# Kernel optimization log

Hardware: AMD Instinct MI355X
Metric: run time of the kernel (lower is better)

The kernel has to match this reference:

```python
import jax, jax.numpy as jnp
import numpy as np

ALPHA = 0.2      # LeakyReLU slope
NFEAT = 128
NHID = 8
NHEADS = 8
BN_EPS = 1e-5


def _xavier(k, shape, gain=1.414):
    fan_in, fan_out = shape[-2], shape[-1]
    lim = gain * np.sqrt(6.0 / (fan_in + fan_out))
    return jax.random.uniform(k, shape, jnp.float32, -lim, lim)


def setup_inputs() -> dict:
    key = jax.random.key(0)
    ks = jax.random.split(key, 10)
    B, N = 32, 512
    return {
        "feats": jax.random.normal(ks[0], (B, NFEAT), jnp.float32),
        "neighbor_feats": jax.random.normal(ks[1], (B, N, NFEAT), jnp.float32),
        # per-head GAT params
        "Ws": _xavier(ks[2], (NHEADS, NFEAT, NHID)),
        "As": _xavier(ks[3], (NHEADS, 2 * NHID, 1)),
        # output GAT layer
        "W_out": _xavier(ks[4], (NHID * NHEADS, NHID)),
        "a_out": _xavier(ks[5], (2 * NHID, 1)),
        # classifier: Linear(nfeat+nhid, nhid) -> PReLU -> BN(eval) -> Linear(nhid, 1)
        "lin1_w": _xavier(ks[6], (NHID, NFEAT + NHID), gain=1.0),
        "lin1_b": jnp.zeros((NHID,), jnp.float32),
        "prelu_a": jnp.array(0.25, jnp.float32),
        "bn_gamma": jnp.ones((NHID,), jnp.float32),
        "bn_beta": jnp.zeros((NHID,), jnp.float32),
        "lin2_w": _xavier(ks[7], (1, NHID), gain=1.0),
        "lin2_b": jnp.zeros((1,), jnp.float32),
    }


def _gat_layer(h, W, a, concat):
    # h: (B,N,F), W: (F,D), a: (2D,1)
    Wh = jnp.einsum('bnf,fd->bnd', h, W)            # (B,N,D)
    D = W.shape[1]
    s1 = Wh @ a[:D, 0]                              # (B,N)  a1 . Wh_i
    s2 = Wh @ a[D:, 0]                              # (B,N)  a2 . Wh_j
    # e[b,i,j] = leakyrelu(s1[b,i] + s2[b,j])  == matmul(cat(Wh_i,Wh_j), a)
    e = jax.nn.leaky_relu(s1[:, :, None] + s2[:, None, :], ALPHA)  # (B,N,N)
    att = jax.nn.softmax(e, axis=1)                 # torch F.softmax(e, dim=1)
    h_prime = jnp.einsum('bij,bjd->bid', att, Wh)   # bmm(attention, Wh)
    return jax.nn.elu(h_prime) if concat else h_prime


def reference(feats, neighbor_feats, Ws, As, W_out, a_out,
              lin1_w, lin1_b, prelu_a, bn_gamma, bn_beta, lin2_w, lin2_b):
    # multi-head GAT (dropout is identity in eval mode)
    heads = jax.vmap(lambda W, a: _gat_layer(neighbor_feats, W, a, True))(Ws, As)  # (H,B,N,D)
    H, B, N, D = heads.shape
    x = jnp.moveaxis(heads, 0, 2).reshape(B, N, H * D)  # concat heads along feature dim
    x = jax.nn.elu(_gat_layer(x, W_out, a_out, False))  # (B,N,NHID)
    gat_feats = x[:, 0]                                 # pooling == 'first'
    z = jnp.concatenate([feats, gat_feats], axis=1)     # (B, NFEAT+NHID)
    z = z @ lin1_w.T + lin1_b
    z = jnp.where(z >= 0, z, prelu_a * z)               # PReLU
    # BatchNorm1d in eval mode with running mean=0, var=1
    z = z / jnp.sqrt(1.0 + BN_EPS) * bn_gamma + bn_beta
    out = z @ lin2_w.T + lin2_b                         # (B,1)
    return out.squeeze(1)
```

## Files before the change

kernel.cpp:

```cpp
#include <hip/hip_runtime.h>
#include <math.h>

#define BB 32
#define NN 512
#define NFEAT 128
#define NHID 8
#define NHEADS 8
#define LALPHA 0.2f

__device__ __forceinline__ float elu1(float x)  { return x > 0.f ? x : __expf(x) - 1.f; }

__device__ __forceinline__ unsigned ordkey(float v) {
    unsigned u = __float_as_uint(v);
    return u ^ (((unsigned)((int)u >> 31)) | 0x80000000u);
}
__device__ __forceinline__ float unord(unsigned k) {
    unsigned u = (k & 0x80000000u) ? (k ^ 0x80000000u) : ~k;
    return __uint_as_float(u);
}

#if __has_builtin(__builtin_amdgcn_update_dpp)
__device__ __forceinline__ float wscan(float x, int lane) {
    int y;
    y = __builtin_amdgcn_update_dpp(0, __float_as_int(x), 0x111, 0xF, 0xF, true); x += __int_as_float(y);
    y = __builtin_amdgcn_update_dpp(0, __float_as_int(x), 0x112, 0xF, 0xF, true); x += __int_as_float(y);
    y = __builtin_amdgcn_update_dpp(0, __float_as_int(x), 0x114, 0xF, 0xF, true); x += __int_as_float(y);
    y = __builtin_amdgcn_update_dpp(0, __float_as_int(x), 0x118, 0xF, 0xF, true); x += __int_as_float(y);
    y = __builtin_amdgcn_update_dpp(0, __float_as_int(x), 0x142, 0xA, 0xF, true); x += __int_as_float(y);
    y = __builtin_amdgcn_update_dpp(0, __float_as_int(x), 0x143, 0xC, 0xF, true); x += __int_as_float(y);
    return x;
}
#else
__device__ __forceinline__ float wscan(float x, int lane) {
    #pragma unroll
    for (int s = 1; s < 64; s <<= 1) {
        float y = __shfl_up(x, (unsigned)s, 64);
        x += (lane >= s) ? y : 0.f;
    }
    return x;
}
#endif

__device__ __forceinline__ unsigned long long shflxor64(unsigned long long x, int j) {
    unsigned lo = (unsigned)__shfl_xor((int)(unsigned)x, j, 64);
    unsigned hw = (unsigned)__shfl_xor((int)(unsigned)(x >> 32), j, 64);
    return (((unsigned long long)hw) << 32) | lo;
}

__device__ __forceinline__ int lb512u64(const unsigned long long* a, unsigned long long v) {
    int lo = 0;
    #pragma unroll
    for (int s = NN / 2; s >= 1; s >>= 1)
        if (a[lo + s - 1] < v) lo += s;
    return lo;
}

__device__ __forceinline__ unsigned long long sortnet512(
        unsigned long long x, unsigned long long* lds, int r, bool active) {
    #pragma unroll
    for (int k = 2; k <= NN; k <<= 1) {
        #pragma unroll
        for (int j = k >> 1; j >= 1; j >>= 1) {
            unsigned long long y;
            if (j >= 64) {
                if (active) lds[r] = x;
                __syncthreads();
                y = active ? lds[r ^ j] : 0ull;
                __syncthreads();
            } else {
                y = shflxor64(x, j);
            }
            if (active) {
                const bool takeMin = ((r & j) == 0) == ((r & k) == 0);
                const bool sw = takeMin ? (y < x) : (x < y);
                x = sw ? y : x;
            }
        }
    }
    if (active) lds[r] = x;
    __syncthreads();
    return x;
}

__global__ __launch_bounds__(1024) void k12_gat1(
        const float* __restrict__ nf, const float* __restrict__ Ws,
        const float* __restrict__ As, float* __restrict__ x)
{
    __shared__ __align__(16) float WT[NHID * NFEAT];
    __shared__ float aL[16];
    __shared__ __align__(16) float whL[NN][NHID];
    __shared__ __align__(16) float part[NN][NHID];
    __shared__ __align__(16) unsigned long long key1L[NN];
    __shared__ __align__(16) unsigned long long key2L[NN];
    __shared__ float prefP[NN], prefQ[NN], denS[NN];
    __shared__ __align__(16) float PP[NN][NHID];
    __shared__ __align__(16) float QQ[NN][NHID];
    __shared__ __align__(16) float wvT[16][NHID];

    const int blk = blockIdx.x;
    const int b = blk & 31, h = blk >> 5;
    const int t = threadIdx.x;
    const int r = t & (NN - 1);
    const bool hi = t >= NN;
    const int lane = t & 63, w = t >> 6;

    {
        const int f = t >> 3, d = t & 7;
        WT[d * NFEAT + f] = Ws[(size_t)h * NFEAT * NHID + t];
    }
    if (t < 16) aL[t] = As[h * 16 + t];
    __syncthreads();

    float acc[NHID];
    {
        #pragma unroll
        for (int d = 0; d < NHID; ++d) acc[d] = 0.f;
        const float4* row = (const float4*)(nf + ((size_t)b * NN + r) * NFEAT + (hi ? 64 : 0));
        const int fb = hi ? 16 : 0;
        const float4* WT4 = (const float4*)WT;
        #pragma unroll 4
        for (int f4 = 0; f4 < 16; ++f4) {
            float4 v = row[f4];
            #pragma unroll
            for (int d = 0; d < NHID; ++d) {
                float4 wv = WT4[d * 32 + fb + f4];
                acc[d] += v.x * wv.x + v.y * wv.y + v.z * wv.z + v.w * wv.w;
            }
        }
        if (hi) {
            float4* pp = (float4*)&part[r][0];
            pp[0] = make_float4(acc[0], acc[1], acc[2], acc[3]);
            pp[1] = make_float4(acc[4], acc[5], acc[6], acc[7]);
        }
    }
    __syncthreads();

    float v1 = 0.f;
    unsigned long long sk = 0ull;
    if (!hi) {
        #pragma unroll
        for (int d = 0; d < NHID; ++d) acc[d] += part[t][d];
        float a1 = 0.f, a2 = 0.f;
        #pragma unroll
        for (int d = 0; d < NHID; ++d) { a1 += acc[d] * aL[d]; a2 += acc[d] * aL[8 + d]; }
        v1 = a1;
        float4* wr = (float4*)&whL[t][0];
        wr[0] = make_float4(acc[0], acc[1], acc[2], acc[3]);
        wr[1] = make_float4(acc[4], acc[5], acc[6], acc[7]);
        sk = (((unsigned long long)ordkey(a1)) << 9) | (unsigned)t;
        key2L[t] = (((unsigned long long)ordkey(a2)) << 9) | (unsigned)t;
    }
    __syncthreads();
    if (hi) sk = key2L[r];

    sk = sortnet512(sk, hi ? key2L : key1L, r, true);

    float ps = 0.f, qs = 0.f;
    float who[NHID];
    float s2r = 0.f, e1p = 0.f, e1q = 0.f;
    int kH = 0, c4 = 0;
    if (!hi) {
        const float s1v = unord((unsigned)(sk >> 9));
        ps = wscan(__expf(s1v), lane);
        qs = wscan(__expf(LALPHA * s1v), lane);
        if (lane == 63) { wvT[w][0] = ps; wvT[w][1] = qs; }
        c4 = lb512u64(key2L, ((unsigned long long)(~ordkey(v1))) << 9);
        e1p = __expf(v1); e1q = __expf(LALPHA * v1);
    } else {
        s2r = unord((unsigned)(sk >> 9));
        const int j = (int)(sk & 511u);
        const float4 w0 = ((const float4*)&whL[j][0])[0];
        const float4 w1 = ((const float4*)&whL[j][0])[1];
        who[0] = w0.x; who[1] = w0.y; who[2] = w0.z; who[3] = w0.w;
        who[4] = w1.x; who[5] = w1.y; who[6] = w1.z; who[7] = w1.w;
        kH = lb512u64(key1L, ((unsigned long long)(~(unsigned)(sk >> 9))) << 9);
    }
    __syncthreads();

    if (!hi) {
        float offp = 0.f, offq = 0.f;
        #pragma unroll
        for (int ww = 0; ww < 8; ++ww) {
            const float tp = wvT[ww][0], tq = wvT[ww][1];
            if (ww < w) { offp += tp; offq += tq; }
        }
        prefP[t] = ps + offp;
        prefQ[t] = qs + offq;
    }
    __syncthreads();

    float pw = 0.f;
    if (hi) {
        const float TPh = prefP[NN - 1];
        const float pk = kH ? prefP[kH - 1] : 0.f;
        const float qk = kH ? prefQ[kH - 1] : 0.f;
        const float den = __expf(s2r) * (TPh - pk) + __expf(LALPHA * s2r) * qk;
        denS[r] = den;
        pw = __expf(LALPHA * s2r) / den;
    } else {
        const unsigned long long k2 = key2L[t];
        const float s2p = unord((unsigned)(k2 >> 9));
        const int j2 = (int)(k2 & 511u);
        const float4 w0 = ((const float4*)&whL[j2][0])[0];
        const float4 w1 = ((const float4*)&whL[j2][0])[1];
        who[0] = w0.x; who[1] = w0.y; who[2] = w0.z; who[3] = w0.w;
        who[4] = w1.x; who[5] = w1.y; who[6] = w1.z; who[7] = w1.w;
        pw = __expf(s2p);
    }
    __syncthreads();

    float pv[NHID];
    if (!hi) pw /= denS[t];
    #pragma unroll
    for (int c = 0; c < NHID; ++c) pv[c] = wscan(pw * who[c], lane);
    if (lane == 63) {
        float4* wp = (float4*)&wvT[w][0];
        wp[0] = make_float4(pv[0], pv[1], pv[2], pv[3]);
        wp[1] = make_float4(pv[4], pv[5], pv[6], pv[7]);
    }
    __syncthreads();

    float tot[NHID];
    {
        const int wb = hi ? 8 : 0;
        float off[NHID];
        #pragma unroll
        for (int c = 0; c < NHID; ++c) { off[c] = 0.f; tot[c] = 0.f; }
        #pragma unroll
        for (int ww = 0; ww < 8; ++ww) {
            const float4 t0 = ((const float4*)&wvT[wb + ww][0])[0];
            const float4 t1 = ((const float4*)&wvT[wb + ww][0])[1];
            tot[0] += t0.x; tot[1] += t0.y; tot[2] += t0.z; tot[3] += t0.w;
            tot[4] += t1.x; tot[5] += t1.y; tot[6] += t1.z; tot[7] += t1.w;
            if (wb + ww < w) {
                off[0] += t0.x; off[1] += t0.y; off[2] += t0.z; off[3] += t0.w;
                off[4] += t1.x; off[5] += t1.y; off[6] += t1.z; off[7] += t1.w;
            }
        }
        #pragma unroll
        for (int c = 0; c < NHID; ++c) pv[c] += off[c];
        float4* dst = hi ? (float4*)&QQ[r][0] : (float4*)&PP[r][0];
        dst[0] = make_float4(pv[0], pv[1], pv[2], pv[3]);
        dst[1] = make_float4(pv[4], pv[5], pv[6], pv[7]);
    }
    __syncthreads();

    if (!hi) {
        float4 P0, P1, Q0, Q1;
        if (c4 > 0) {
            const float4* pp4 = (const float4*)&PP[c4 - 1][0];
            const float4* qq4 = (const float4*)&QQ[c4 - 1][0];
            P0 = pp4[0]; P1 = pp4[1]; Q0 = qq4[0]; Q1 = qq4[1];
        } else {
            P0 = P1 = Q0 = Q1 = make_float4(0.f, 0.f, 0.f, 0.f);
        }
        float h0 = e1p * (tot[0] - P0.x) + e1q * Q0.x;
        float h1 = e1p * (tot[1] - P0.y) + e1q * Q0.y;
        float h2 = e1p * (tot[2] - P0.z) + e1q * Q0.z;
        float h3 = e1p * (tot[3] - P0.w) + e1q * Q0.w;
        float h4 = e1p * (tot[4] - P1.x) + e1q * Q1.x;
        float h5 = e1p * (tot[5] - P1.y) + e1q * Q1.y;
        float h6 = e1p * (tot[6] - P1.z) + e1q * Q1.z;
        float h7 = e1p * (tot[7] - P1.w) + e1q * Q1.w;
        float* xp = x + ((size_t)(b * NN + t)) * (NHEADS * NHID) + h * NHID;
        ((float4*)xp)[0] = make_float4(elu1(h0), elu1(h1), elu1(h2), elu1(h3));
        ((float4*)xp)[1] = make_float4(elu1(h4), elu1(h5), elu1(h6), elu1(h7));
    }
}

__global__ __launch_bounds__(1024) void k34_tail(
        const float* __restrict__ x, const float* __restrict__ Wout,
        const float* __restrict__ aout, const float* __restrict__ feats,
        const float* __restrict__ l1w, const float* __restrict__ l1b,
        const float* __restrict__ pa, const float* __restrict__ gma,
        const float* __restrict__ bta, const float* __restrict__ l2w,
        const float* __restrict__ l2b, float* __restrict__ out)
{
    __shared__ __align__(16) float WLT[NHID * 64];
    __shared__ float aL[16];
    __shared__ __align__(16) float wh2[NN][NHID];
    __shared__ __align__(16) float part[NN][NHID];
    __shared__ __align__(16) unsigned long long key1L[NN];
    __shared__ float s2L[NN];
    __shared__ float prefP[NN], prefQ[NN];
    __shared__ float wvT[8][2];
    __shared__ float wR[8][NHID];
    __shared__ float hp[2][NHID];
    __shared__ float gatL[NHID];
    __shared__ float zL[NHID];
    __shared__ float s1zero;

    const int b = blockIdx.x, t = threadIdx.x;
    const int r = t & (NN - 1);
    const bool hi = t >= NN;
    const int lane = t & 63, w = t >> 6;

    if (t < 512) {
        const int f = t >> 3, d = t & 7;
        WLT[d * 64 + f] = Wout[t];
    }
    if (t < 16) aL[t] = aout[t];
    __syncthreads();

    float acc[NHID];
    {
        #pragma unroll
        for (int d = 0; d < NHID; ++d) acc[d] = 0.f;
        const float4* row = (const float4*)(x + ((size_t)b * NN + r) * (NHEADS * NHID) + (hi ? 32 : 0));
        const int fb = hi ? 8 : 0;
        const float4* WT4 = (const float4*)WLT;
        #pragma unroll 4
        for (int f4 = 0; f4 < 8; ++f4) {
            float4 v = row[f4];
            #pragma unroll
            for (int d = 0; d < NHID; ++d) {
                float4 wv = WT4[d * 16 + fb + f4];
                acc[d] += v.x * wv.x + v.y * wv.y + v.z * wv.z + v.w * wv.w;
            }
        }
        if (hi) {
            float4* pp = (float4*)&part[r][0];
            pp[0] = make_float4(acc[0], acc[1], acc[2], acc[3]);
            pp[1] = make_float4(acc[4], acc[5], acc[6], acc[7]);
        }
    }
    __syncthreads();

    unsigned long long sk = 0ull;
    if (!hi) {
        #pragma unroll
        for (int d = 0; d < NHID; ++d) acc[d] += part[t][d];
        float a1 = 0.f, a2 = 0.f;
        #pragma unroll
        for (int d = 0; d < NHID; ++d) { a1 += acc[d] * aL[d]; a2 += acc[d] * aL[8 + d]; }
        float4* wr = (float4*)&wh2[t][0];
        wr[0] = make_float4(acc[0], acc[1], acc[2], acc[3]);
        wr[1] = make_float4(acc[4], acc[5], acc[6], acc[7]);
        sk = (((unsigned long long)ordkey(a1)) << 9) | (unsigned)t;
        s2L[t] = a2;
        if (t == 0) s1zero = a1;
    }
    __syncthreads();

    sk = sortnet512(sk, key1L, r, !hi);

    float ps = 0.f, qs = 0.f;
    int c3 = 0; float v2h = 0.f;
    if (!hi) {
        const float s1v = unord((unsigned)(sk >> 9));
        ps = wscan(__expf(s1v), lane);
        qs = wscan(__expf(LALPHA * s1v), lane);
        if (lane == 63) { wvT[w][0] = ps; wvT[w][1] = qs; }
    } else {
        v2h = s2L[r];
        c3 = lb512u64(key1L, ((unsigned long long)(~ordkey(v2h))) << 9);
    }
    __syncthreads();

    if (!hi) {
        float offp = 0.f, offq = 0.f;
        #pragma unroll
        for (int ww = 0; ww < 8; ++ww) {
            const float tp = wvT[ww][0], tq = wvT[ww][1];
            if (ww < w) { offp += tp; offq += tq; }
        }
        prefP[t] = ps + offp;
        prefQ[t] = qs + offq;
    }
    __syncthreads();

    if (hi) {
        const float TPh = prefP[NN - 1];
        const float pk = c3 ? prefP[c3 - 1] : 0.f;
        const float qk = c3 ? prefQ[c3 - 1] : 0.f;
        const float dj = __expf(v2h) * (TPh - pk) + __expf(LALPHA * v2h) * qk;
        float e0 = s1zero + v2h;
        e0 = e0 >= 0.f ? e0 : LALPHA * e0;
        const float wgt = __expf(e0) / dj;
        float a[NHID];
        const float4 q0 = ((const float4*)&wh2[r][0])[0];
        const float4 q1 = ((const float4*)&wh2[r][0])[1];
        a[0] = wgt * q0.x; a[1] = wgt * q0.y; a[2] = wgt * q0.z; a[3] = wgt * q0.w;
        a[4] = wgt * q1.x; a[5] = wgt * q1.y; a[6] = wgt * q1.z; a[7] = wgt * q1.w;
        #pragma unroll
        for (int s = 1; s < 64; s <<= 1) {
            #pragma unroll
            for (int d = 0; d < NHID; ++d) a[d] += __shfl_xor(a[d], s, 64);
        }
        if (lane == 0) {
            #pragma unroll
            for (int d = 0; d < NHID; ++d) wR[w - 8][d] = a[d];
        }
    } else if (t < 128) {
        const float fk = feats[b * NFEAT + t];
        #pragma unroll
        for (int d = 0; d < NHID; ++d) {
            float p = fk * l1w[d * (NFEAT + NHID) + t];
            #pragma unroll
            for (int s = 1; s < 64; s <<= 1) p += __shfl_xor(p, s, 64);
            if (lane == 0) hp[w][d] = p;
        }
    }
    __syncthreads();

    if (t < NHID) {
        float g = 0.f;
        #pragma unroll
        for (int ww = 0; ww < 8; ++ww) g += wR[ww][t];
        gatL[t] = elu1(g);
    }
    __syncthreads();

    if (t < NHID) {
        const float* wv = l1w + t * (NFEAT + NHID);
        float z = l1b[t] + hp[0][t] + hp[1][t];
        #pragma unroll
        for (int k = 0; k < NHID; ++k) z += gatL[k] * wv[NFEAT + k];
        const float a = pa[0];
        z = z >= 0.f ? z : a * z;
        z = z * (1.f / sqrtf(1.f + 1e-5f)) * gma[t] + bta[t];
        zL[t] = z;
    }
    __syncthreads();
    if (t == 0) {
        float o = l2b[0];
        #pragma unroll
        for (int d = 0; d < NHID; ++d) o += zL[d] * l2w[d];
        out[b] = o;
    }
}

extern "C" void kernel_launch(void* const* d_in, const int* in_sizes, int n_in,
                              void* d_out, int out_size, void* d_ws, size_t ws_size,
                              hipStream_t stream) {
    const float* feats = (const float*)d_in[0];
    const float* nf    = (const float*)d_in[1];
    const float* Ws    = (const float*)d_in[2];
    const float* As    = (const float*)d_in[3];
    const float* Wout  = (const float*)d_in[4];
    const float* aout  = (const float*)d_in[5];
    const float* l1w   = (const float*)d_in[6];
    const float* l1b   = (const float*)d_in[7];
    const float* pa    = (const float*)d_in[8];
    const float* gma   = (const float*)d_in[9];
    const float* bta   = (const float*)d_in[10];
    const float* l2w   = (const float*)d_in[11];
    const float* l2b   = (const float*)d_in[12];
    float* out = (float*)d_out;

    float* x = (float*)d_ws;

    k12_gat1<<<BB * NHEADS, 1024, 0, stream>>>(nf, Ws, As, x);
    k34_tail<<<BB, 1024, 0, stream>>>(x, Wout, aout, feats, l1w, l1b, pa, gma, bta, l2w, l2b, out);
}
```

Measured before the change: 40.16 us.

## Replace block-wide bitonic sort with per-wave sort plus merge-by-rank

Replaces the 512-element bitonic network, which needed many block-wide barriers for strides of 64 and above, with a 64-lane in-wave bitonic sort, one LDS write of the sorted runs, and a scatter where each element finds its global rank by binary search in the other seven runs. The goal is to cut the many __syncthreads rounds in both GAT kernels. The price is extra LDS arrays and 7 binary searches per element. Some exponentials are also computed one phase earlier, one barrier phase is merged, and the classifier partial dot products in the second kernel are moved into the idle high half of the block during the sort.

Result: no change. 39.78 us (median of 2 runs) (-1.0%).

```diff
diff --git a/kernel.cpp b/kernel.cpp
--- a/kernel.cpp
+++ b/kernel.cpp
@@ -47,39 +47,46 @@
     return (((unsigned long long)hw) << 32) | lo;
 }
 
-__device__ __forceinline__ int lb512u64(const unsigned long long* a, unsigned long long v) {
+__device__ __forceinline__ unsigned long long wsort64(unsigned long long x, int lane) {
+    #pragma unroll
+    for (int k = 2; k <= 64; k <<= 1) {
+        #pragma unroll
+        for (int j = k >> 1; j >= 1; j >>= 1) {
+            unsigned long long y = shflxor64(x, j);
+            const bool takeMin = ((lane & j) == 0) == ((lane & k) == 0);
+            const bool sw = takeMin ? (y < x) : (x < y);
+            x = sw ? y : x;
+        }
+    }
+    return x;
+}
+
+__device__ __forceinline__ int lb64u(const unsigned long long* a, unsigned long long v) {
     int lo = 0;
     #pragma unroll
-    for (int s = NN / 2; s >= 1; s >>= 1)
-        if (a[lo + s - 1] < v) lo += s;
+    for (int s = 64; s >= 1; s >>= 1) {
+        const int i2 = lo + s - 1;
+        if (i2 < 64 && a[i2] < v) lo += s;
+    }
     return lo;
 }
-
-__device__ __forceinline__ unsigned long long sortnet512(
-        unsigned long long x, unsigned long long* lds, int r, bool active) {
-    #pragma unroll
-    for (int k = 2; k <= NN; k <<= 1) {
-        #pragma unroll
-        for (int j = k >> 1; j >= 1; j >>= 1) {
-            unsigned long long y;
-            if (j >= 64) {
-                if (active) lds[r] = x;
-                __syncthreads();
-                y = active ? lds[r ^ j] : 0ull;
-                __syncthreads();
-            } else {
-                y = shflxor64(x, j);
-            }
-            if (active) {
-                const bool takeMin = ((r & j) == 0) == ((r & k) == 0);
-                const bool sw = takeMin ? (y < x) : (x < y);
-                x = sw ? y : x;
-            }
-        }
-    }
-    if (active) lds[r] = x;
-    __syncthreads();
-    return x;
+__device__ __forceinline__ int lb512u(const unsigned long long* a, unsigned long long v) {
+    int lo = 0;
+    #pragma unroll
+    for (int s = NN; s >= 1; s >>= 1) {
+        const int i2 = lo + s - 1;
+        if (i2 < NN && a[i2] < v) lo += s;
+    }
+    return lo;
+}
+
+__device__ __forceinline__ int rank512(const unsigned long long* runs, unsigned long long x,
+                                       int wr, int lane) {
+    int rk = lane;
+    #pragma unroll
+    for (int w2 = 0; w2 < 8; ++w2)
+        if (w2 != wr) rk += lb64u(runs + 64 * w2, x);
+    return rk;
 }
 
 __global__ __launch_bounds__(1024) void k12_gat1(
@@ -92,6 +99,8 @@
     __shared__ __align__(16) float part[NN][NHID];
     __shared__ __align__(16) unsigned long long key1L[NN];
     __shared__ __align__(16) unsigned long long key2L[NN];
+    __shared__ __align__(16) unsigned long long keyR1[NN];
+    __shared__ __align__(16) unsigned long long keyR2[NN];
     __shared__ float prefP[NN], prefQ[NN], denS[NN];
     __shared__ __align__(16) float PP[NN][NHID];
     __shared__ __align__(16) float QQ[NN][NHID];
@@ -103,6 +112,7 @@
     const int r = t & (NN - 1);
     const bool hi = t >= NN;
     const int lane = t & 63, w = t >> 6;
+    const int wr = w & 7;
 
     {
         const int f = t >> 3, d = t & 7;
@@ -144,39 +154,51 @@
         #pragma unroll
         for (int d = 0; d < NHID; ++d) { a1 += acc[d] * aL[d]; a2 += acc[d] * aL[8 + d]; }
         v1 = a1;
-        float4* wr = (float4*)&whL[t][0];
-        wr[0] = make_float4(acc[0], acc[1], acc[2], acc[3]);
-        wr[1] = make_float4(acc[4], acc[5], acc[6], acc[7]);
+        float4* wrp = (float4*)&whL[t][0];
+        wrp[0] = make_float4(acc[0], acc[1], acc[2], acc[3]);
+        wrp[1] = make_float4(acc[4], acc[5], acc[6], acc[7]);
         sk = (((unsigned long long)ordkey(a1)) << 9) | (unsigned)t;
         key2L[t] = (((unsigned long long)ordkey(a2)) << 9) | (unsigned)t;
     }
     __syncthreads();
+
     if (hi) sk = key2L[r];
-
-    sk = sortnet512(sk, hi ? key2L : key1L, r, true);
+    sk = wsort64(sk, lane);
+    if (!hi) keyR1[t] = sk; else keyR2[r] = sk;
+    __syncthreads();
+
+    {
+        const unsigned long long* runs = hi ? keyR2 : keyR1;
+        const int rk = rank512(runs, sk, wr, lane);
+        if (!hi) key1L[rk] = sk; else key2L[rk] = sk;
+    }
+    __syncthreads();
 
     float ps = 0.f, qs = 0.f;
     float who[NHID];
-    float s2r = 0.f, e1p = 0.f, e1q = 0.f;
+    float s2r = 0.f, e2p = 0.f, e2q = 0.f, e1p = 0.f, e1q = 0.f;
     int kH = 0, c4 = 0;
     if (!hi) {
-        const float s1v = unord((unsigned)(sk >> 9));
+        const float s1v = unord((unsigned)(key1L[t] >> 9));
         ps = wscan(__expf(s1v), lane);
         qs = wscan(__expf(LALPHA * s1v), lane);
         if (lane == 63) { wvT[w][0] = ps; wvT[w][1] = qs; }
-        c4 = lb512u64(key2L, ((unsigned long long)(~ordkey(v1))) << 9);
+        c4 = lb512u(key2L, ((unsigned long long)(~ordkey(v1))) << 9);
         e1p = __expf(v1); e1q = __expf(LALPHA * v1);
     } else {
-        s2r = unord((unsigned)(sk >> 9));
-        const int j = (int)(sk & 511u);
+        const unsigned long long k2 = key2L[r];
+        s2r = unord((unsigned)(k2 >> 9));
+        const int j = (int)(k2 & 511u);
         const float4 w0 = ((const float4*)&whL[j][0])[0];
         const float4 w1 = ((const float4*)&whL[j][0])[1];
         who[0] = w0.x; who[1] = w0.y; who[2] = w0.z; who[3] = w0.w;
         who[4] = w1.x; who[5] = w1.y; who[6] = w1.z; who[7] = w1.w;
-        kH = lb512u64(key1L, ((unsigned long long)(~(unsigned)(sk >> 9))) << 9);
-    }
-    __syncthreads();
-
+        kH = lb512u(key1L, ((unsigned long long)(~(unsigned)(k2 >> 9))) << 9);
+        e2p = __expf(s2r); e2q = __expf(LALPHA * s2r);
+    }
+    __syncthreads();
+
+    float pw = 0.f;
     if (!hi) {
         float offp = 0.f, offq = 0.f;
         #pragma unroll
@@ -186,18 +208,6 @@
         }
         prefP[t] = ps + offp;
         prefQ[t] = qs + offq;
-    }
-    __syncthreads();
-
-    float pw = 0.f;
-    if (hi) {
-        const float TPh = prefP[NN - 1];
-        const float pk = kH ? prefP[kH - 1] : 0.f;
-        const float qk = kH ? prefQ[kH - 1] : 0.f;
-        const float den = __expf(s2r) * (TPh - pk) + __expf(LALPHA * s2r) * qk;
-        denS[r] = den;
-        pw = __expf(LALPHA * s2r) / den;
-    } else {
         const unsigned long long k2 = key2L[t];
         const float s2p = unord((unsigned)(k2 >> 9));
         const int j2 = (int)(k2 & 511u);
@@ -206,6 +216,16 @@
         who[0] = w0.x; who[1] = w0.y; who[2] = w0.z; who[3] = w0.w;
         who[4] = w1.x; who[5] = w1.y; who[6] = w1.z; who[7] = w1.w;
         pw = __expf(s2p);
+    }
+    __syncthreads();
+
+    if (hi) {
+        const float TPh = prefP[NN - 1];
+        const float pk = kH ? prefP[kH - 1] : 0.f;
+        const float qk = kH ? prefQ[kH - 1] : 0.f;
+        const float den = e2p * (TPh - pk) + e2q * qk;
+        denS[r] = den;
+        pw = e2q / den;
     }
     __syncthreads();
 
@@ -281,6 +301,7 @@
     __shared__ __align__(16) float wh2[NN][NHID];
     __shared__ __align__(16) float part[NN][NHID];
     __shared__ __align__(16) unsigned long long key1L[NN];
+    __shared__ __align__(16) unsigned long long keyR1[NN];
     __shared__ float s2L[NN];
     __shared__ float prefP[NN], prefQ[NN];
     __shared__ float wvT[8][2];
@@ -294,6 +315,7 @@
     const int r = t & (NN - 1);
     const bool hi = t >= NN;
     const int lane = t & 63, w = t >> 6;
+    const int wr = w & 7;
 
     if (t < 512) {
         const int f = t >> 3, d = t & 7;
@@ -333,27 +355,47 @@
         float a1 = 0.f, a2 = 0.f;
         #pragma unroll
         for (int d = 0; d < NHID; ++d) { a1 += acc[d] * aL[d]; a2 += acc[d] * aL[8 + d]; }
-        float4* wr = (float4*)&wh2[t][0];
-        wr[0] = make_float4(acc[0], acc[1], acc[2], acc[3]);
-        wr[1] = make_float4(acc[4], acc[5], acc[6], acc[7]);
+        float4* wrp = (float4*)&wh2[t][0];
+        wrp[0] = make_float4(acc[0], acc[1], acc[2], acc[3]);
+        wrp[1] = make_float4(acc[4], acc[5], acc[6], acc[7]);
         sk = (((unsigned long long)ordkey(a1)) << 9) | (unsigned)t;
         s2L[t] = a2;
         if (t == 0) s1zero = a1;
     }
     __syncthreads();
 
-    sk = sortnet512(sk, key1L, r, !hi);
+    if (!hi) {
+        sk = wsort64(sk, lane);
+        keyR1[t] = sk;
+    } else if (r < 128) {
+        const float fk = feats[b * NFEAT + r];
+        #pragma unroll
+        for (int d = 0; d < NHID; ++d) {
+            float p = fk * l1w[d * (NFEAT + NHID) + r];
+            #pragma unroll
+            for (int s = 1; s < 64; s <<= 1) p += __shfl_xor(p, s, 64);
+            if (lane == 0) hp[w - 8][d] = p;
+        }
+    }
+    __syncthreads();
+
+    if (!hi) {
+        const int rk = rank512(keyR1, sk, wr, lane);
+        key1L[rk] = sk;
+    }
+    __syncthreads();
 
     float ps = 0.f, qs = 0.f;
-    int c3 = 0; float v2h = 0.f;
-    if (!hi) {
-        const float s1v = unord((unsigned)(sk >> 9));
+    int c3 = 0; float v2h = 0.f, e2p = 0.f, e2q = 0.f;
+    if (!hi) {
+        const float s1v = unord((unsigned)(key1L[t] >> 9));
         ps = wscan(__expf(s1v), lane);
         qs = wscan(__expf(LALPHA * s1v), lane);
         if (lane == 63) { wvT[w][0] = ps; wvT[w][1] = qs; }
     } else {
         v2h = s2L[r];
-        c3 = lb512u64(key1L, ((unsigned long long)(~ordkey(v2h))) << 9);
+        c3 = lb512u(key1L, ((unsigned long long)(~ordkey(v2h))) << 9);
+        e2p = __expf(v2h); e2q = __expf(LALPHA * v2h);
     }
     __syncthreads();
 
@@ -373,7 +415,7 @@
         const float TPh = prefP[NN - 1];
         const float pk = c3 ? prefP[c3 - 1] : 0.f;
         const float qk = c3 ? prefQ[c3 - 1] : 0.f;
-        const float dj = __expf(v2h) * (TPh - pk) + __expf(LALPHA * v2h) * qk;
+        const float dj = e2p * (TPh - pk) + e2q * qk;
         float e0 = s1zero + v2h;
         e0 = e0 >= 0.f ? e0 : LALPHA * e0;
         const float wgt = __expf(e0) / dj;
@@ -390,15 +432,6 @@
         if (lane == 0) {
             #pragma unroll
             for (int d = 0; d < NHID; ++d) wR[w - 8][d] = a[d];
-        }
-    } else if (t < 128) {
-        const float fk = feats[b * NFEAT + t];
-        #pragma unroll
-        for (int d = 0; d < NHID; ++d) {
-            float p = fk * l1w[d * (NFEAT + NHID) + t];
-            #pragma unroll
-            for (int s = 1; s < 64; s <<= 1) p += __shfl_xor(p, s, 64);
-            if (lane == 0) hp[w][d] = p;
         }
     }
     __syncthreads();
```
